# Kernel tuning notes

Hardware: AMD Instinct MI355X
Metric: run time of the kernel (lower is better)

## Reference

```python
import jax, jax.numpy as jnp
import numpy as np

NQ, NT, D = 2048, 131072, 64   # query nodes, target nodes, feature dim
E = 2_000_000                  # candidate (u, v) edges
M = 1024                       # consensus (nn_map) pairs; vc = top M rows of Xt


def setup_inputs() -> dict:
    key = jax.random.key(0)
    ks = jax.random.split(key, 8)
    Xq = jax.random.normal(ks[0], (NQ, D), dtype=jnp.float32)
    Xt = jax.random.normal(ks[1], (NT, D), dtype=jnp.float32)
    W_alpha = jax.random.normal(ks[2], (D, D), dtype=jnp.float32) * 0.05
    b_alpha = jax.random.normal(ks[3], (1,), dtype=jnp.float32) * 0.05
    W_beta = jax.random.normal(ks[4], (D, D), dtype=jnp.float32) * 0.05
    b_beta = jax.random.normal(ks[5], (1,), dtype=jnp.float32) * 0.05
    u_idx = jax.random.randint(ks[6], (E,), 0, NQ, dtype=jnp.int32)
    # candidate targets live in [0, NT - M); consensus targets in [NT - M, NT)
    v_idx = jax.random.randint(ks[7], (E,), 0, NT - M, dtype=jnp.int32)
    uc = jax.random.randint(jax.random.fold_in(key, 7), (M,), 0, NQ, dtype=jnp.int32)
    vc = (NT - M) + jnp.arange(M, dtype=jnp.int32)
    return {"Xq": Xq, "Xt": Xt, "W_alpha": W_alpha, "b_alpha": b_alpha,
            "W_beta": W_beta, "b_beta": b_beta,
            "u_idx": u_idx, "v_idx": v_idx, "uc": uc, "vc": vc}


def reference(Xq, Xt, W_alpha, b_alpha, W_beta, b_beta, u_idx, v_idx, uc, vc):
    # 1) consensus overwrite: Xt[vc] = Xq[uc]  (nn_map)
    Xt_c = Xt.at[vc].set(Xq[uc])

    # 2) per-edge gather + bilinear interaction scoring
    xq_e = Xq[u_idx]      # [E, D]
    xt_e = Xt_c[v_idx]    # [E, D]

    def bilinear(W, b):
        return jnp.einsum('ed,df,ef->e', xq_e, W, xt_e) + b[0]

    beta = jax.nn.sigmoid(bilinear(W_beta, b_beta))   # [E] gate
    alpha = jax.nn.elu(bilinear(W_alpha, b_alpha))    # [E] score
    h_e = (1.0 - beta)[:, None] * xq_e + beta[:, None] * xt_e  # [E, D]

    # 3) segment softmax over incoming u per target v (== masked softmax over Nq)
    m = jax.ops.segment_max(alpha, v_idx, num_segments=NT)     # -inf on empty segments
    a = jnp.exp(alpha - m[v_idx])
    s = jax.ops.segment_sum(a, v_idx, num_segments=NT)
    a = a / s[v_idx] + 1e-10   # matches original +1e-10 after normalization

    # 4) scatter-aggregate weighted messages back into Xt rows with >=1 candidate
    agg = jax.ops.segment_sum(a[:, None] * h_e, v_idx, num_segments=NT)  # [NT, D]
    deg = jax.ops.segment_sum(jnp.ones_like(alpha), v_idx, num_segments=NT)
    Xt_out = jnp.where((deg > 0)[:, None], agg, Xt_c)
    return (Xq, Xt_out)
```

## Files before the change

### kernel.cpp

```cpp
#include <hip/hip_runtime.h>

#define NQ 2048
#define NT 131072
#define DD 64
#define MM 1024
#define NBUCK 512
#define BCAP 4608
#define CHUNK 4096

__global__ void yq_kernel(const float* __restrict__ Xq,
                          const float* __restrict__ Wa,
                          const float* __restrict__ Wb,
                          float* __restrict__ Yqa,
                          float* __restrict__ Yqb) {
    int r = blockIdx.x * 4 + (threadIdx.x >> 6);
    int j = threadIdx.x & 63;
    float sa = 0.f, sb = 0.f;
#pragma unroll
    for (int k = 0; k < DD; ++k) {
        float x = Xq[r * DD + k];
        sa = fmaf(x, Wa[k * DD + j], sa);
        sb = fmaf(x, Wb[k * DD + j], sb);
    }
    Yqa[r * DD + j] = sa;
    Yqb[r * DD + j] = sb;
}

__global__ __launch_bounds__(256) void bin_kernel(
        const int* __restrict__ u_idx, const int* __restrict__ v_idx,
        int* __restrict__ gcur, unsigned* __restrict__ gbuf, int E) {
    __shared__ unsigned pk[CHUNK];
    __shared__ unsigned stage[CHUNK];
    __shared__ int hist[NBUCK], off[NBUCK], base[NBUCK], cur[NBUCK];
    __shared__ int tmp[256];
    int tid = threadIdx.x;
    int e0 = blockIdx.x * CHUNK;
    int n = min(CHUNK, E - e0);
    if (n <= 0) return;

    for (int i = tid; i < NBUCK; i += 256) hist[i] = 0;
    __syncthreads();
    for (int i = tid; i < n; i += 256) {
        unsigned u = (unsigned)u_idx[e0 + i];
        unsigned v = (unsigned)v_idx[e0 + i];
        unsigned p = (v << 11) | u;
        pk[i] = p;
        atomicAdd(&hist[p >> 19], 1);
    }
    __syncthreads();
    int h0 = hist[2 * tid], h1 = hist[2 * tid + 1];
    int pairsum = h0 + h1;
    tmp[tid] = pairsum;
    __syncthreads();
    for (int d = 1; d < 256; d <<= 1) {
        int y = (tid >= d) ? tmp[tid - d] : 0;
        __syncthreads();
        tmp[tid] += y;
        __syncthreads();
    }
    int excl = tmp[tid] - pairsum;
    off[2 * tid] = excl;
    off[2 * tid + 1] = excl + h0;
    __syncthreads();
    for (int i = tid; i < NBUCK; i += 256) {
        base[i] = hist[i] ? atomicAdd(&gcur[i], hist[i]) : 0;
        cur[i] = off[i];
    }
    __syncthreads();
    for (int i = tid; i < n; i += 256) {
        unsigned p = pk[i];
        int pos = atomicAdd(&cur[p >> 19], 1);
        stage[pos] = p;
    }
    __syncthreads();
    for (int i = tid; i < n; i += 256) {
        unsigned p = stage[i];
        int b = p >> 19;
        int idx = base[b] + (i - off[b]);
        if (idx < BCAP) gbuf[(size_t)b * BCAP + idx] = p;
    }
}

#define DOT4(a, b) fmaf((a).x, (b).x, fmaf((a).y, (b).y, fmaf((a).z, (b).z, (a).w * (b).w)))

__global__ __launch_bounds__(1024, 8) void bucket_kernel(
        const float* __restrict__ Xq,
        const float* __restrict__ Xt,
        const float* __restrict__ Yqa,
        const float* __restrict__ Yqb,
        const float* __restrict__ ba,
        const float* __restrict__ bb,
        const int* __restrict__ gcur,
        const unsigned* __restrict__ gbuf,
        const int* __restrict__ uc,
        float* __restrict__ outXt) {
    __shared__ unsigned pk[BCAP];
    __shared__ unsigned short su[BCAP];
    __shared__ int hist[256], cur[256], rstart[257];
    int tid = threadIdx.x;
    int b = blockIdx.x;
    int n = min(gcur[b], BCAP);

    if (tid < 256) hist[tid] = 0;
    __syncthreads();
    for (int i = tid; i < n; i += 1024) {
        unsigned p = gbuf[(size_t)b * BCAP + i];
        pk[i] = p;
        atomicAdd(&hist[(p >> 11) & 255], 1);
    }
    __syncthreads();
    if (tid < 64) {
        int h0 = hist[4 * tid], h1 = hist[4 * tid + 1];
        int h2 = hist[4 * tid + 2], h3 = hist[4 * tid + 3];
        int tot = h0 + h1 + h2 + h3;
        int incl = tot;
#pragma unroll
        for (int d = 1; d < 64; d <<= 1) {
            int y = __shfl_up(incl, d, 64);
            if (tid >= d) incl += y;
        }
        int excl = incl - tot;
        rstart[4 * tid] = excl;
        rstart[4 * tid + 1] = excl + h0;
        rstart[4 * tid + 2] = excl + h0 + h1;
        rstart[4 * tid + 3] = excl + h0 + h1 + h2;
        cur[4 * tid] = excl;
        cur[4 * tid + 1] = excl + h0;
        cur[4 * tid + 2] = excl + h0 + h1;
        cur[4 * tid + 3] = excl + h0 + h1 + h2;
        if (tid == 63) rstart[256] = excl + tot;
    }
    __syncthreads();
    for (int i = tid; i < n; i += 1024) {
        unsigned p = pk[i];
        int pos = atomicAdd(&cur[(p >> 11) & 255], 1);
        su[pos] = (unsigned short)(p & 0x7FFu);
    }
    __syncthreads();

    int lane = tid & 63;
    int w = tid >> 6;
    int l16 = lane & 15;
    int g = lane >> 4;
    float ba0 = ba[0], bb0 = bb[0];

    for (int r = w; r < 256; r += 16) {
        int v = (b << 8) + r;
        int startr = rstart[r];
        int deg = rstart[r + 1] - startr;
        float4 xt4 = ((const float4*)(Xt + (size_t)v * DD))[l16];
        if (deg == 0) {
            if (g == 0) {
                float4 o = xt4;
                if (v >= NT - MM) {
                    int u = uc[v - (NT - MM)];
                    o = ((const float4*)(Xq + (size_t)u * DD))[l16];
                }
                ((float4*)(outXt + (size_t)v * DD))[l16] = o;
            }
            continue;
        }
        float4 acc = make_float4(0.f, 0.f, 0.f, 0.f);
        float4 hsum = make_float4(0.f, 0.f, 0.f, 0.f);
        float s = 0.f;
        int k = g;
        for (; k + 4 < deg; k += 8) {
            int u0 = (int)su[startr + k];
            int u1 = (int)su[startr + k + 4];
            float4 ya0 = ((const float4*)(Yqa + u0 * DD))[l16];
            float4 yb0 = ((const float4*)(Yqb + u0 * DD))[l16];
            float4 ya1 = ((const float4*)(Yqa + u1 * DD))[l16];
            float4 yb1 = ((const float4*)(Yqb + u1 * DD))[l16];
            float pa0 = DOT4(ya0, xt4), pb0 = DOT4(yb0, xt4);
            float pa1 = DOT4(ya1, xt4), pb1 = DOT4(yb1, xt4);
#pragma unroll
            for (int off = 1; off < 16; off <<= 1) {
                pa0 += __shfl_xor(pa0, off, 64);
                pb0 += __shfl_xor(pb0, off, 64);
                pa1 += __shfl_xor(pa1, off, 64);
                pb1 += __shfl_xor(pb1, off, 64);
            }
            float la0 = pa0 + ba0, la1 = pa1 + ba0;
            float al0 = la0 > 0.f ? la0 : (__expf(la0) - 1.f);
            float al1 = la1 > 0.f ? la1 : (__expf(la1) - 1.f);
            float a0 = __expf(al0), a1 = __expf(al1);
            float be0 = __builtin_amdgcn_rcpf(1.f + __expf(-(pb0 + bb0)));
            float be1 = __builtin_amdgcn_rcpf(1.f + __expf(-(pb1 + bb0)));
            float4 xq0 = ((const float4*)(Xq + u0 * DD))[l16];
            float4 xq1 = ((const float4*)(Xq + u1 * DD))[l16];
            float4 h0, h1;
            h0.x = fmaf(be0, xt4.x - xq0.x, xq0.x);
            h0.y = fmaf(be0, xt4.y - xq0.y, xq0.y);
            h0.z = fmaf(be0, xt4.z - xq0.z, xq0.z);
            h0.w = fmaf(be0, xt4.w - xq0.w, xq0.w);
            h1.x = fmaf(be1, xt4.x - xq1.x, xq1.x);
            h1.y = fmaf(be1, xt4.y - xq1.y, xq1.y);
            h1.z = fmaf(be1, xt4.z - xq1.z, xq1.z);
            h1.w = fmaf(be1, xt4.w - xq1.w, xq1.w);
            acc.x = fmaf(a0, h0.x, fmaf(a1, h1.x, acc.x));
            acc.y = fmaf(a0, h0.y, fmaf(a1, h1.y, acc.y));
            acc.z = fmaf(a0, h0.z, fmaf(a1, h1.z, acc.z));
            acc.w = fmaf(a0, h0.w, fmaf(a1, h1.w, acc.w));
            hsum.x += h0.x + h1.x; hsum.y += h0.y + h1.y;
            hsum.z += h0.z + h1.z; hsum.w += h0.w + h1.w;
            s += a0 + a1;
        }
        if (k < deg) {
            int u = (int)su[startr + k];
            float4 ya = ((const float4*)(Yqa + u * DD))[l16];
            float4 yb = ((const float4*)(Yqb + u * DD))[l16];
            float pa = DOT4(ya, xt4), pb = DOT4(yb, xt4);
#pragma unroll
            for (int off = 1; off < 16; off <<= 1) {
                pa += __shfl_xor(pa, off, 64);
                pb += __shfl_xor(pb, off, 64);
            }
            float la = pa + ba0;
            float al = la > 0.f ? la : (__expf(la) - 1.f);
            float a = __expf(al);
            float be = __builtin_amdgcn_rcpf(1.f + __expf(-(pb + bb0)));
            float4 xq = ((const float4*)(Xq + u * DD))[l16];
            float4 h;
            h.x = fmaf(be, xt4.x - xq.x, xq.x);
            h.y = fmaf(be, xt4.y - xq.y, xq.y);
            h.z = fmaf(be, xt4.z - xq.z, xq.z);
            h.w = fmaf(be, xt4.w - xq.w, xq.w);
            acc.x = fmaf(a, h.x, acc.x);
            acc.y = fmaf(a, h.y, acc.y);
            acc.z = fmaf(a, h.z, acc.z);
            acc.w = fmaf(a, h.w, acc.w);
            hsum.x += h.x; hsum.y += h.y; hsum.z += h.z; hsum.w += h.w;
            s += a;
        }
#pragma unroll
        for (int off = 16; off < 64; off <<= 1) {
            acc.x += __shfl_xor(acc.x, off, 64);
            acc.y += __shfl_xor(acc.y, off, 64);
            acc.z += __shfl_xor(acc.z, off, 64);
            acc.w += __shfl_xor(acc.w, off, 64);
            hsum.x += __shfl_xor(hsum.x, off, 64);
            hsum.y += __shfl_xor(hsum.y, off, 64);
            hsum.z += __shfl_xor(hsum.z, off, 64);
            hsum.w += __shfl_xor(hsum.w, off, 64);
            s += __shfl_xor(s, off, 64);
        }
        if (g == 0) {
            float inv = __builtin_amdgcn_rcpf(s);
            float4 o;
            o.x = fmaf(acc.x, inv, 1e-10f * hsum.x);
            o.y = fmaf(acc.y, inv, 1e-10f * hsum.y);
            o.z = fmaf(acc.z, inv, 1e-10f * hsum.z);
            o.w = fmaf(acc.w, inv, 1e-10f * hsum.w);
            ((float4*)(outXt + (size_t)v * DD))[l16] = o;
        }
    }
}

extern "C" void kernel_launch(void* const* d_in, const int* in_sizes, int n_in,
                              void* d_out, int out_size, void* d_ws, size_t ws_size,
                              hipStream_t stream) {
    const float* Xq = (const float*)d_in[0];
    const float* Xt = (const float*)d_in[1];
    const float* Wa = (const float*)d_in[2];
    const float* ba = (const float*)d_in[3];
    const float* Wb = (const float*)d_in[4];
    const float* bb = (const float*)d_in[5];
    const int* u_idx = (const int*)d_in[6];
    const int* v_idx = (const int*)d_in[7];
    const int* uc = (const int*)d_in[8];
    const int* vc = (const int*)d_in[9];
    const int E = in_sizes[6];
    (void)vc;

    float* out = (float*)d_out;
    float* outXq = out;
    float* outXt = out + NQ * DD;

    char* ws = (char*)d_ws;
    float* Yqa = (float*)ws;          ws += NQ * DD * sizeof(float);
    float* Yqb = (float*)ws;          ws += NQ * DD * sizeof(float);
    int* gcur = (int*)ws;             ws += NBUCK * sizeof(int);
    ws = (char*)(((size_t)ws + 255) & ~(size_t)255);
    unsigned* gbuf = (unsigned*)ws;   ws += (size_t)NBUCK * BCAP * sizeof(unsigned);

    hipMemcpyAsync(outXq, Xq, NQ * DD * sizeof(float), hipMemcpyDeviceToDevice, stream);
    hipMemsetAsync(gcur, 0, NBUCK * sizeof(int), stream);

    yq_kernel<<<NQ / 4, 256, 0, stream>>>(Xq, Wa, Wb, Yqa, Yqb);

    int nchunks = (E + CHUNK - 1) / CHUNK;
    bin_kernel<<<nchunks, 256, 0, stream>>>(u_idx, v_idx, gcur, gbuf, E);

    bucket_kernel<<<NBUCK, 1024, 0, stream>>>(Xq, Xt, Yqa, Yqb, ba, bb, gcur, gbuf,
                                              uc, outXt);
}
```

Measured before the change: 236.3 us.

## Restructure binning with 1024-thread vectorized loads and assign one target row per quarter-wave

The bin kernel now runs 1024 threads that each load four edges with int4 vector loads and keep them in registers, which removes the pk shared staging array and replaces the block-wide scan with a wave-shuffle scan. The bucket kernel drops its shared pk copy and reads gbuf twice instead. Each 16-lane group now handles a whole target row serially, which removes the cross-group shuffle reduction. The 1e-10*hsum correction term is dropped and the ELU exp is computed unconditionally. This trades per-row parallelism and a small numeric term for less reduction and synchronisation overhead, and load imbalance across rows with different degrees may increase.

After: 220.0 us. -6.9%, faster.

```diff
diff --git a/kernel.cpp b/kernel.cpp
--- a/kernel.cpp
+++ b/kernel.cpp
@@ -26,64 +26,76 @@
     Yqb[r * DD + j] = sb;
 }
 
-__global__ __launch_bounds__(256) void bin_kernel(
+__global__ __launch_bounds__(1024) void bin_kernel(
         const int* __restrict__ u_idx, const int* __restrict__ v_idx,
         int* __restrict__ gcur, unsigned* __restrict__ gbuf, int E) {
-    __shared__ unsigned pk[CHUNK];
     __shared__ unsigned stage[CHUNK];
     __shared__ int hist[NBUCK], off[NBUCK], base[NBUCK], cur[NBUCK];
-    __shared__ int tmp[256];
     int tid = threadIdx.x;
     int e0 = blockIdx.x * CHUNK;
     int n = min(CHUNK, E - e0);
     if (n <= 0) return;
 
-    for (int i = tid; i < NBUCK; i += 256) hist[i] = 0;
-    __syncthreads();
-    for (int i = tid; i < n; i += 256) {
-        unsigned u = (unsigned)u_idx[e0 + i];
-        unsigned v = (unsigned)v_idx[e0 + i];
-        unsigned p = (v << 11) | u;
-        pk[i] = p;
-        atomicAdd(&hist[p >> 19], 1);
-    }
-    __syncthreads();
-    int h0 = hist[2 * tid], h1 = hist[2 * tid + 1];
-    int pairsum = h0 + h1;
-    tmp[tid] = pairsum;
-    __syncthreads();
-    for (int d = 1; d < 256; d <<= 1) {
-        int y = (tid >= d) ? tmp[tid - d] : 0;
-        __syncthreads();
-        tmp[tid] += y;
-        __syncthreads();
-    }
-    int excl = tmp[tid] - pairsum;
-    off[2 * tid] = excl;
-    off[2 * tid + 1] = excl + h0;
-    __syncthreads();
-    for (int i = tid; i < NBUCK; i += 256) {
+    for (int i = tid; i < NBUCK; i += 1024) hist[i] = 0;
+    __syncthreads();
+
+    unsigned p[4];
+    int nv = 0;
+    int i0 = tid * 4;
+    if (i0 + 3 < n) {
+        int4 u4 = *(const int4*)(u_idx + e0 + i0);
+        int4 v4 = *(const int4*)(v_idx + e0 + i0);
+        p[0] = ((unsigned)v4.x << 11) | (unsigned)u4.x;
+        p[1] = ((unsigned)v4.y << 11) | (unsigned)u4.y;
+        p[2] = ((unsigned)v4.z << 11) | (unsigned)u4.z;
+        p[3] = ((unsigned)v4.w << 11) | (unsigned)u4.w;
+        nv = 4;
+    } else {
+        for (int j = 0; j < 4; ++j) {
+            if (i0 + j < n) {
+                p[j] = ((unsigned)v_idx[e0 + i0 + j] << 11) | (unsigned)u_idx[e0 + i0 + j];
+                ++nv;
+            }
+        }
+    }
+    for (int j = 0; j < nv; ++j) atomicAdd(&hist[p[j] >> 19], 1);
+    __syncthreads();
+    if (tid < 64) {
+        int h[8], sum = 0;
+#pragma unroll
+        for (int j = 0; j < 8; ++j) { h[j] = hist[8 * tid + j]; sum += h[j]; }
+        int incl = sum;
+#pragma unroll
+        for (int d = 1; d < 64; d <<= 1) {
+            int y = __shfl_up(incl, d, 64);
+            if (tid >= d) incl += y;
+        }
+        int excl = incl - sum;
+#pragma unroll
+        for (int j = 0; j < 8; ++j) { off[8 * tid + j] = excl; excl += h[j]; }
+    }
+    __syncthreads();
+    for (int i = tid; i < NBUCK; i += 1024) {
         base[i] = hist[i] ? atomicAdd(&gcur[i], hist[i]) : 0;
         cur[i] = off[i];
     }
     __syncthreads();
-    for (int i = tid; i < n; i += 256) {
-        unsigned p = pk[i];
-        int pos = atomicAdd(&cur[p >> 19], 1);
-        stage[pos] = p;
-    }
-    __syncthreads();
-    for (int i = tid; i < n; i += 256) {
-        unsigned p = stage[i];
-        int b = p >> 19;
+    for (int j = 0; j < nv; ++j) {
+        int pos = atomicAdd(&cur[p[j] >> 19], 1);
+        stage[pos] = p[j];
+    }
+    __syncthreads();
+    for (int i = tid; i < n; i += 1024) {
+        unsigned q = stage[i];
+        int b = q >> 19;
         int idx = base[b] + (i - off[b]);
-        if (idx < BCAP) gbuf[(size_t)b * BCAP + idx] = p;
+        if (idx < BCAP) gbuf[(size_t)b * BCAP + idx] = q;
     }
 }
 
 #define DOT4(a, b) fmaf((a).x, (b).x, fmaf((a).y, (b).y, fmaf((a).z, (b).z, (a).w * (b).w)))
 
-__global__ __launch_bounds__(1024, 8) void bucket_kernel(
+__global__ __launch_bounds__(1024, 2) void bucket_kernel(
         const float* __restrict__ Xq,
         const float* __restrict__ Xt,
         const float* __restrict__ Yqa,
@@ -94,7 +106,6 @@
         const unsigned* __restrict__ gbuf,
         const int* __restrict__ uc,
         float* __restrict__ outXt) {
-    __shared__ unsigned pk[BCAP];
     __shared__ unsigned short su[BCAP];
     __shared__ int hist[256], cur[256], rstart[257];
     int tid = threadIdx.x;
@@ -103,11 +114,8 @@
 
     if (tid < 256) hist[tid] = 0;
     __syncthreads();
-    for (int i = tid; i < n; i += 1024) {
-        unsigned p = gbuf[(size_t)b * BCAP + i];
-        pk[i] = p;
-        atomicAdd(&hist[(p >> 11) & 255], 1);
-    }
+    for (int i = tid; i < n; i += 1024)
+        atomicAdd(&hist[(gbuf[(size_t)b * BCAP + i] >> 11) & 255], 1);
     __syncthreads();
     if (tid < 64) {
         int h0 = hist[4 * tid], h1 = hist[4 * tid + 1];
@@ -120,19 +128,15 @@
             if (tid >= d) incl += y;
         }
         int excl = incl - tot;
-        rstart[4 * tid] = excl;
-        rstart[4 * tid + 1] = excl + h0;
-        rstart[4 * tid + 2] = excl + h0 + h1;
-        rstart[4 * tid + 3] = excl + h0 + h1 + h2;
-        cur[4 * tid] = excl;
-        cur[4 * tid + 1] = excl + h0;
-        cur[4 * tid + 2] = excl + h0 + h1;
-        cur[4 * tid + 3] = excl + h0 + h1 + h2;
+        rstart[4 * tid] = excl;             cur[4 * tid] = excl;
+        rstart[4 * tid + 1] = excl + h0;    cur[4 * tid + 1] = excl + h0;
+        rstart[4 * tid + 2] = excl + h0 + h1;      cur[4 * tid + 2] = excl + h0 + h1;
+        rstart[4 * tid + 3] = excl + h0 + h1 + h2; cur[4 * tid + 3] = excl + h0 + h1 + h2;
         if (tid == 63) rstart[256] = excl + tot;
     }
     __syncthreads();
     for (int i = tid; i < n; i += 1024) {
-        unsigned p = pk[i];
+        unsigned p = gbuf[(size_t)b * BCAP + i];
         int pos = atomicAdd(&cur[(p >> 11) & 255], 1);
         su[pos] = (unsigned short)(p & 0x7FFu);
     }
@@ -142,31 +146,31 @@
     int w = tid >> 6;
     int l16 = lane & 15;
     int g = lane >> 4;
+    int gid = w * 4 + g;
     float ba0 = ba[0], bb0 = bb[0];
 
-    for (int r = w; r < 256; r += 16) {
+    for (int r = gid; r < 256; r += 64) {
         int v = (b << 8) + r;
         int startr = rstart[r];
         int deg = rstart[r + 1] - startr;
+        if (deg == 0) {
+            float4 o;
+            if (v >= NT - MM) {
+                int u = uc[v - (NT - MM)];
+                o = ((const float4*)(Xq + (size_t)u * DD))[l16];
+            } else {
+                o = ((const float4*)(Xt + (size_t)v * DD))[l16];
+            }
+            ((float4*)(outXt + (size_t)v * DD))[l16] = o;
+            continue;
+        }
         float4 xt4 = ((const float4*)(Xt + (size_t)v * DD))[l16];
-        if (deg == 0) {
-            if (g == 0) {
-                float4 o = xt4;
-                if (v >= NT - MM) {
-                    int u = uc[v - (NT - MM)];
-                    o = ((const float4*)(Xq + (size_t)u * DD))[l16];
-                }
-                ((float4*)(outXt + (size_t)v * DD))[l16] = o;
-            }
-            continue;
-        }
         float4 acc = make_float4(0.f, 0.f, 0.f, 0.f);
-        float4 hsum = make_float4(0.f, 0.f, 0.f, 0.f);
         float s = 0.f;
-        int k = g;
-        for (; k + 4 < deg; k += 8) {
+        int k = 0;
+        for (; k + 1 < deg; k += 2) {
             int u0 = (int)su[startr + k];
-            int u1 = (int)su[startr + k + 4];
+            int u1 = (int)su[startr + k + 1];
             float4 ya0 = ((const float4*)(Yqa + u0 * DD))[l16];
             float4 yb0 = ((const float4*)(Yqb + u0 * DD))[l16];
             float4 ya1 = ((const float4*)(Yqa + u1 * DD))[l16];
@@ -181,8 +185,9 @@
                 pb1 += __shfl_xor(pb1, off, 64);
             }
             float la0 = pa0 + ba0, la1 = pa1 + ba0;
-            float al0 = la0 > 0.f ? la0 : (__expf(la0) - 1.f);
-            float al1 = la1 > 0.f ? la1 : (__expf(la1) - 1.f);
+            float t0 = __expf(la0), t1 = __expf(la1);
+            float al0 = la0 > 0.f ? la0 : (t0 - 1.f);
+            float al1 = la1 > 0.f ? la1 : (t1 - 1.f);
             float a0 = __expf(al0), a1 = __expf(al1);
             float be0 = __builtin_amdgcn_rcpf(1.f + __expf(-(pb0 + bb0)));
             float be1 = __builtin_amdgcn_rcpf(1.f + __expf(-(pb1 + bb0)));
@@ -201,8 +206,6 @@
             acc.y = fmaf(a0, h0.y, fmaf(a1, h1.y, acc.y));
             acc.z = fmaf(a0, h0.z, fmaf(a1, h1.z, acc.z));
             acc.w = fmaf(a0, h0.w, fmaf(a1, h1.w, acc.w));
-            hsum.x += h0.x + h1.x; hsum.y += h0.y + h1.y;
-            hsum.z += h0.z + h1.z; hsum.w += h0.w + h1.w;
             s += a0 + a1;
         }
         if (k < deg) {
@@ -216,43 +219,20 @@
                 pb += __shfl_xor(pb, off, 64);
             }
             float la = pa + ba0;
-            float al = la > 0.f ? la : (__expf(la) - 1.f);
+            float t = __expf(la);
+            float al = la > 0.f ? la : (t - 1.f);
             float a = __expf(al);
             float be = __builtin_amdgcn_rcpf(1.f + __expf(-(pb + bb0)));
             float4 xq = ((const float4*)(Xq + u * DD))[l16];
-            float4 h;
-            h.x = fmaf(be, xt4.x - xq.x, xq.x);
-            h.y = fmaf(be, xt4.y - xq.y, xq.y);
-            h.z = fmaf(be, xt4.z - xq.z, xq.z);
-            h.w = fmaf(be, xt4.w - xq.w, xq.w);
-            acc.x = fmaf(a, h.x, acc.x);
-            acc.y = fmaf(a, h.y, acc.y);
-            acc.z = fmaf(a, h.z, acc.z);
-            acc.w = fmaf(a, h.w, acc.w);
-            hsum.x += h.x; hsum.y += h.y; hsum.z += h.z; hsum.w += h.w;
+            acc.x = fmaf(a, fmaf(be, xt4.x - xq.x, xq.x), acc.x);
+            acc.y = fmaf(a, fmaf(be, xt4.y - xq.y, xq.y), acc.y);
+            acc.z = fmaf(a, fmaf(be, xt4.z - xq.z, xq.z), acc.z);
+            acc.w = fmaf(a, fmaf(be, xt4.w - xq.w, xq.w), acc.w);
             s += a;
         }
-#pragma unroll
-        for (int off = 16; off < 64; off <<= 1) {
-            acc.x += __shfl_xor(acc.x, off, 64);
-            acc.y += __shfl_xor(acc.y, off, 64);
-            acc.z += __shfl_xor(acc.z, off, 64);
-            acc.w += __shfl_xor(acc.w, off, 64);
-            hsum.x += __shfl_xor(hsum.x, off, 64);
-            hsum.y += __shfl_xor(hsum.y, off, 64);
-            hsum.z += __shfl_xor(hsum.z, off, 64);
-            hsum.w += __shfl_xor(hsum.w, off, 64);
-            s += __shfl_xor(s, off, 64);
-        }
-        if (g == 0) {
-            float inv = __builtin_amdgcn_rcpf(s);
-            float4 o;
-            o.x = fmaf(acc.x, inv, 1e-10f * hsum.x);
-            o.y = fmaf(acc.y, inv, 1e-10f * hsum.y);
-            o.z = fmaf(acc.z, inv, 1e-10f * hsum.z);
-            o.w = fmaf(acc.w, inv, 1e-10f * hsum.w);
-            ((float4*)(outXt + (size_t)v * DD))[l16] = o;
-        }
+        float inv = __builtin_amdgcn_rcpf(s);
+        float4 o = make_float4(acc.x * inv, acc.y * inv, acc.z * inv, acc.w * inv);
+        ((float4*)(outXt + (size_t)v * DD))[l16] = o;
     }
 }
 
@@ -289,7 +269,7 @@
     yq_kernel<<<NQ / 4, 256, 0, stream>>>(Xq, Wa, Wb, Yqa, Yqb);
 
     int nchunks = (E + CHUNK - 1) / CHUNK;
-    bin_kernel<<<nchunks, 256, 0, stream>>>(u_idx, v_idx, gcur, gbuf, E);
+    bin_kernel<<<nchunks, 1024, 0, stream>>>(u_idx, v_idx, gcur, gbuf, E);
 
     bucket_kernel<<<NBUCK, 1024, 0, stream>>>(Xq, Xt, Yqa, Yqb, ba, bb, gcur, gbuf,
                                               uc, outXt);
```
